# Optimization experiments

Hardware: AMD Instinct MI355X
Metric: run time of the kernel (lower is better)

The kernel has to match this reference:

```python
import jax, jax.numpy as jnp
import numpy as np
from jax import lax

EPS = 1e-5
NF, NH, HD = 1024, 2, 2  # num_features, heads, head_size (hidden_size=4)


def _prelu(x, a):
    return jnp.where(x >= 0, x, a * x)


def _bn2d(x, g, b):  # training-mode BatchNorm2d over (N,H,W)
    m = x.mean(axis=(0, 2, 3), keepdims=True)
    v = ((x - m) ** 2).mean(axis=(0, 2, 3), keepdims=True)
    return (x - m) / jnp.sqrt(v + EPS) * g[None, :, None, None] + b[None, :, None, None]


def _bn1d(x, g, b):  # training-mode BatchNorm1d over batch
    m = x.mean(axis=0, keepdims=True)
    v = ((x - m) ** 2).mean(axis=0, keepdims=True)
    return (x - m) / jnp.sqrt(v + EPS) * g + b


def _ln(x, g, b):
    m = x.mean(axis=-1, keepdims=True)
    v = ((x - m) ** 2).mean(axis=-1, keepdims=True)
    return (x - m) / jnp.sqrt(v + EPS) * g + b


def _conv(x, w, b, stride):
    y = lax.conv_general_dilated(x, w, window_strides=stride, padding='VALID',
                                 dimension_numbers=('NCHW', 'OIHW', 'NCHW'))
    return y + b[None, :, None, None]


def setup_inputs() -> dict:
    key = jax.random.key(0)
    ks = jax.random.split(key, 24)
    r = lambda i, shape, s=0.05: jax.random.normal(ks[i], shape, jnp.float32) * s
    ones = lambda n: jnp.ones((n,), jnp.float32)
    zeros = lambda n: jnp.zeros((n,), jnp.float32)
    return {
        'vertex_pos': r(0, (32, 3), 1.0),
        'body_mesh': r(1, (32, 20813, 3), 1.0),
        'conv1_w': r(2, (3, 1, 409, 3)), 'conv1_b': r(3, (3,)),
        'bn1_g': ones(3), 'bn1_b': zeros(3),
        'conv2_w': r(4, (3, 1, 330, 3)), 'conv2_b': r(5, (3,)),
        'bn2_g': ones(3), 'bn2_b': zeros(3),
        'prelu_a': jnp.float32(0.25),
        'wq': r(6, (4, 9)), 'bq': r(7, (4,)),
        'wk': r(8, (4, 9)), 'bk': r(9, (4,)),
        'wv': r(10, (4, 9)), 'bv': r(11, (4,)),
        'fc_w': r(12, (1024, 4096)), 'fc_b': r(13, (1024,)),
        'ff1_w': r(14, (1024, 1024)), 'ff1_b': r(15, (1024,)),
        'ln_g': ones(1024), 'ln_b': zeros(1024),
        'ff2_w': r(16, (48, 1024)), 'ff2_b': r(17, (48,)),
        'fus_w0': r(18, (48, 32, 3)), 'fus_b0': r(19, (48, 32)),
        'fus_w1': r(20, (48, 128, 32)), 'fus_b1': r(21, (48, 128)),
        'bnf0_g': ones(32), 'bnf0_b': zeros(32),
        'bnf1_g': ones(128), 'bnf1_b': zeros(128),
        'prelu_f': jnp.float32(0.25),
        'out_w': r(22, (1, 128)), 'out_b': r(23, (1,)),
    }


def reference(vertex_pos, body_mesh, conv1_w, conv1_b, bn1_g, bn1_b, conv2_w, conv2_b,
              bn2_g, bn2_b, prelu_a, wq, bq, wk, bk, wv, bv, fc_w, fc_b,
              ff1_w, ff1_b, ln_g, ln_b, ff2_w, ff2_b,
              fus_w0, fus_b0, fus_w1, fus_b1, bnf0_g, bnf0_b, bnf1_g, bnf1_b,
              prelu_f, out_w, out_b):
    B = vertex_pos.shape[0]
    # --- mesh encoder (MultiHeadAttention_conv.mesh_encoder) ---
    mesh = body_mesh.reshape(B, 1, -1, 3)                             # [B,1,20813,3]
    x = _bn2d(_conv(mesh, conv1_w, conv1_b, (6, 1)), bn1_g, bn1_b)    # [B,3,3401,1]
    x = x.reshape(B, 1, -1, 3)                                        # [B,1,3401,3]
    x = _bn2d(_conv(x, conv2_w, conv2_b, (1, 1)), bn2_g, bn2_b)       # [B,3,3072,1]
    x = _prelu(x.reshape(B, NF, -1), prelu_a)                         # [B,1024,9]
    # --- multi-head attention ---
    def heads(t):  # [B,NF,NH*HD] -> [B,NH,NF,HD]
        return t.reshape(B, NF, NH, HD).transpose(0, 2, 1, 3)
    q = heads(x @ wq.T + bq)
    k = heads(x @ wk.T + bk)
    v = heads(x @ wv.T + bv)
    scores = jnp.einsum('bhqd,bhkd->bhqk', q, k) / (HD ** 0.5)        # [B,2,1024,1024]
    attn = jax.nn.softmax(scores, axis=-1)
    av = jnp.einsum('bhqk,bhkd->bhqd', attn, v)
    av = av.transpose(0, 2, 1, 3).reshape(B, NF * NH * HD)            # [B,4096]
    h = av @ fc_w.T + fc_b                                            # [B,1024]
    # --- GMW feed-forward (residual) + motion weights ---
    h = h + jax.nn.elu(_ln(h @ ff1_w.T + ff1_b, ln_g, ln_b))
    mw = h @ ff2_w.T + ff2_b                                          # [B,48]
    w = mw / jnp.sum(mw, axis=1, keepdims=True)                       # normalized gates
    # --- fused MoE stage: 48 experts per depth, batched as one grouped GEMM ---
    s = vertex_pos.reshape(B, 3)
    for We, be, g, bb in ((fus_w0, fus_b0, bnf0_g, bnf0_b),
                          (fus_w1, fus_b1, bnf1_g, bnf1_b)):
        y = jnp.einsum('eoi,bi->beo', We, s) + be[None]               # [B,48,out]
        s = jnp.einsum('beo,be->bo', y, w)                            # gated sum over experts
        s = _prelu(_bn1d(s, g, bb), prelu_f)
    return jax.nn.sigmoid(s @ out_w.T + out_b)                        # [B,1]
```

## Files before the change

### kernel.cpp

```cpp
#include <hip/hip_runtime.h>

#define EPSF 1e-5f

__device__ __forceinline__ float wred(float v) {
#pragma unroll
  for (int off = 32; off > 0; off >>= 1) v += __shfl_down(v, off, 64);
  return v;
}

__global__ __launch_bounds__(256) void k_conv1(
    const float* __restrict__ mesh, const float* __restrict__ cw,
    const float* __restrict__ cb, float* __restrict__ out,
    float* __restrict__ part) {
  __shared__ float wsm[3684];
  __shared__ float sm[3513];
  __shared__ float pm[384];
  __shared__ float redm[4][6];
  const int tid = threadIdx.x;
  const int tile = blockIdx.x % 27, b = blockIdx.x / 27;
  const int oh0 = tile << 7;
  const int nvalid = min(128, 3401 - oh0);
  const int nload = (nvalid - 1) * 18 + 1227;
  for (int j = tid; j < 3681; j += 256) {
    int c = (j >= 2454) ? 2 : ((j >= 1227) ? 1 : 0);
    wsm[c * 1228 + (j - c * 1227)] = cw[j];
  }
  const float* src = mesh + b * 62439 + oh0 * 18;
  for (int j = tid; j < nload; j += 256) sm[j] = src[j];
  __syncthreads();
  const int half = tid >> 7, oidx = tid & 127;
  const float* xp = sm + oidx * 18;
  const int i0 = half ? 614 : 0, i1 = half ? 1226 : 614;
  float a0 = 0.f, a1 = 0.f, a2 = 0.f;
#pragma unroll 4
  for (int i = i0; i < i1; i += 2) {
    float2 x = *(const float2*)(xp + i);
    float2 w0 = *(const float2*)(wsm + i);
    float2 w1 = *(const float2*)(wsm + 1228 + i);
    float2 w2 = *(const float2*)(wsm + 2456 + i);
    a0 = fmaf(w0.x, x.x, fmaf(w0.y, x.y, a0));
    a1 = fmaf(w1.x, x.x, fmaf(w1.y, x.y, a1));
    a2 = fmaf(w2.x, x.x, fmaf(w2.y, x.y, a2));
  }
  if (half) {
    float x = xp[1226];
    a0 = fmaf(wsm[1226], x, a0);
    a1 = fmaf(wsm[1228 + 1226], x, a1);
    a2 = fmaf(wsm[2456 + 1226], x, a2);
    pm[oidx] = a0; pm[128 + oidx] = a1; pm[256 + oidx] = a2;
  }
  __syncthreads();
  float st[6] = {0.f, 0.f, 0.f, 0.f, 0.f, 0.f};
  if (!half && oidx < nvalid) {
    a0 += pm[oidx] + cb[0];
    a1 += pm[128 + oidx] + cb[1];
    a2 += pm[256 + oidx] + cb[2];
    float* op = out + b * 10203 + oh0 + oidx;
    op[0] = a0; op[3401] = a1; op[6802] = a2;
    st[0] = a0; st[1] = a0 * a0; st[2] = a1; st[3] = a1 * a1; st[4] = a2; st[5] = a2 * a2;
  }
  const int lane = tid & 63, wid = tid >> 6;
#pragma unroll
  for (int c = 0; c < 6; ++c) {
    float rv = wred(st[c]);
    if (lane == 0) redm[wid][c] = rv;
  }
  __syncthreads();
  if (tid < 6)
    part[blockIdx.x * 6 + tid] = redm[0][tid] + redm[1][tid] + redm[2][tid] + redm[3][tid];
}

__global__ __launch_bounds__(256) void k_conv2(
    const float* __restrict__ x1, const float* __restrict__ part1,
    const float* __restrict__ g1, const float* __restrict__ be1,
    const float* __restrict__ cw, const float* __restrict__ cb,
    float* __restrict__ out, float* __restrict__ part) {
  __shared__ float wsm[2970];
  __shared__ float sm[1371];
  __shared__ float pm[384];
  __shared__ float redm[4][6];
  __shared__ float coef[6];
  const int tid = threadIdx.x;
  const int lane = tid & 63, wid = tid >> 6;
  {
    float r[6] = {0.f, 0.f, 0.f, 0.f, 0.f, 0.f};
    for (int j = tid; j < 864; j += 256) {
#pragma unroll
      for (int c = 0; c < 6; ++c) r[c] += part1[j * 6 + c];
    }
#pragma unroll
    for (int c = 0; c < 6; ++c) {
      float rv = wred(r[c]);
      if (lane == 0) redm[wid][c] = rv;
    }
    __syncthreads();
    if (tid == 0) {
      const float inv_n = 1.f / (32.f * 3401.f);
#pragma unroll
      for (int c = 0; c < 3; ++c) {
        float s = redm[0][2 * c] + redm[1][2 * c] + redm[2][2 * c] + redm[3][2 * c];
        float ss = redm[0][2 * c + 1] + redm[1][2 * c + 1] + redm[2][2 * c + 1] + redm[3][2 * c + 1];
        float m = s * inv_n;
        float var = ss * inv_n - m * m;
        float a = g1[c] * rsqrtf(var + EPSF);
        coef[c] = a; coef[3 + c] = be1[c] - m * a;
      }
    }
  }
  for (int j = tid; j < 2970; j += 256) wsm[j] = cw[j];
  __syncthreads();
  const int tile = blockIdx.x % 24, b = blockIdx.x / 24;
  const int oh0 = tile << 7;
  const int g0 = oh0 * 3;
  const float* src = x1 + b * 10203 + g0;
  for (int j = tid; j < 1371; j += 256) {
    int gg = g0 + j;
    int c = (gg >= 6802) ? 2 : ((gg >= 3401) ? 1 : 0);
    sm[j] = fmaf(coef[c], src[j], coef[3 + c]);
  }
  __syncthreads();
  const int half = tid >> 7, oidx = tid & 127;
  const float* xp = sm + oidx * 3;
  const int i0 = half ? 496 : 0, i1 = half ? 990 : 496;
  float a0 = 0.f, a1 = 0.f, a2 = 0.f;
#pragma unroll 4
  for (int i = i0; i < i1; i += 2) {
    float x0 = xp[i], x1v = xp[i + 1];
    float2 w0 = *(const float2*)(wsm + i);
    float2 w1 = *(const float2*)(wsm + 990 + i);
    float2 w2 = *(const float2*)(wsm + 1980 + i);
    a0 = fmaf(w0.x, x0, fmaf(w0.y, x1v, a0));
    a1 = fmaf(w1.x, x0, fmaf(w1.y, x1v, a1));
    a2 = fmaf(w2.x, x0, fmaf(w2.y, x1v, a2));
  }
  if (half) { pm[oidx] = a0; pm[128 + oidx] = a1; pm[256 + oidx] = a2; }
  __syncthreads();
  float st[6] = {0.f, 0.f, 0.f, 0.f, 0.f, 0.f};
  if (!half) {
    a0 += pm[oidx] + cb[0];
    a1 += pm[128 + oidx] + cb[1];
    a2 += pm[256 + oidx] + cb[2];
    float* op = out + b * 9216 + oh0 + oidx;
    op[0] = a0; op[3072] = a1; op[6144] = a2;
    st[0] = a0; st[1] = a0 * a0; st[2] = a1; st[3] = a1 * a1; st[4] = a2; st[5] = a2 * a2;
  }
  __syncthreads();
#pragma unroll
  for (int c = 0; c < 6; ++c) {
    float rv = wred(st[c]);
    if (lane == 0) redm[wid][c] = rv;
  }
  __syncthreads();
  if (tid < 6)
    part[blockIdx.x * 6 + tid] = redm[0][tid] + redm[1][tid] + redm[2][tid] + redm[3][tid];
}

__global__ __launch_bounds__(256) void k_qkv(
    const float* __restrict__ x2, const float* __restrict__ part2,
    const float* __restrict__ g2, const float* __restrict__ be2,
    const float* __restrict__ pa_p,
    const float* __restrict__ wq, const float* __restrict__ bq,
    const float* __restrict__ wk, const float* __restrict__ bk,
    const float* __restrict__ wv, const float* __restrict__ bv,
    float* __restrict__ qo, float* __restrict__ ko, float* __restrict__ vo) {
  __shared__ float redm[4][6];
  __shared__ float coef[6];
  const int tid = threadIdx.x;
  const int lane = tid & 63, wid = tid >> 6;
  {
    float r[6] = {0.f, 0.f, 0.f, 0.f, 0.f, 0.f};
    for (int j = tid; j < 768; j += 256) {
#pragma unroll
      for (int c = 0; c < 6; ++c) r[c] += part2[j * 6 + c];
    }
#pragma unroll
    for (int c = 0; c < 6; ++c) {
      float rv = wred(r[c]);
      if (lane == 0) redm[wid][c] = rv;
    }
    __syncthreads();
    if (tid == 0) {
      const float inv_n = 1.f / (32.f * 3072.f);
#pragma unroll
      for (int c = 0; c < 3; ++c) {
        float s = redm[0][2 * c] + redm[1][2 * c] + redm[2][2 * c] + redm[3][2 * c];
        float ss = redm[0][2 * c + 1] + redm[1][2 * c + 1] + redm[2][2 * c + 1] + redm[3][2 * c + 1];
        float m = s * inv_n;
        float var = ss * inv_n - m * m;
        float a = g2[c] * rsqrtf(var + EPSF);
        coef[c] = a; coef[3 + c] = be2[c] - m * a;
      }
    }
    __syncthreads();
  }
  const float pa = pa_p[0];
  const int id = blockIdx.x * 256 + tid;
  const int b = id >> 10, f = id & 1023;
  const float* src = x2 + b * 9216 + f * 9;
  float x[9];
  const int z0 = f * 9;
#pragma unroll
  for (int j = 0; j < 9; ++j) {
    int z = z0 + j;
    int c = (z >= 6144) ? 2 : ((z >= 3072) ? 1 : 0);
    float v = fmaf(coef[c], src[j], coef[3 + c]);
    x[j] = (v >= 0.f) ? v : pa * v;
  }
  const float QSCALE = 0.70710678118654752f * 1.44269504088896341f;
#pragma unroll
  for (int dd = 0; dd < 4; ++dd) {
    float q = bq[dd], k = bk[dd], v = bv[dd];
#pragma unroll
    for (int j = 0; j < 9; ++j) {
      q = fmaf(wq[dd * 9 + j], x[j], q);
      k = fmaf(wk[dd * 9 + j], x[j], k);
      v = fmaf(wv[dd * 9 + j], x[j], v);
    }
    int hh = dd >> 1, d = dd & 1;
    int idx = ((b * 2 + hh) * 1024 + f) * 2 + d;
    qo[idx] = q * QSCALE;
    ko[idx] = k;
    vo[idx] = v;
  }
}

__device__ __forceinline__ int kvIdx(int j) { return j + (j >> 7); }

__global__ __launch_bounds__(256) void k_attn(
    const float* __restrict__ q, const float* __restrict__ k,
    const float* __restrict__ v, float* __restrict__ av) {
  __shared__ float4 kv[1032];
  __shared__ float smax[4];
  const int tid = threadIdx.x;
  const int bh = blockIdx.x >> 3, rblk = blockIdx.x & 7;
  const float2* kp = (const float2*)(k + bh * 2048);
  const float2* vp = (const float2*)(v + bh * 2048);
  float nkm = 0.f;
  for (int j = tid; j < 1024; j += 256) {
    float2 kk = kp[j], vv = vp[j];
    kv[kvIdx(j)] = make_float4(kk.x, kk.y, vv.x, vv.y);
    nkm = fmaxf(nkm, fmaf(kk.x, kk.x, kk.y * kk.y));
  }
#pragma unroll
  for (int off = 32; off > 0; off >>= 1) nkm = fmaxf(nkm, __shfl_xor(nkm, off, 64));
  if ((tid & 63) == 0) smax[tid >> 6] = nkm;
  __syncthreads();
  const float knorm = sqrtf(fmaxf(fmaxf(smax[0], smax[1]), fmaxf(smax[2], smax[3])));
  const int lane = tid & 63, w = tid >> 6;
  const int rg = (w << 3) | (lane >> 3);
  const int ks = lane & 7;
  const int r0 = rblk * 128 + rg * 4;
  const float4 q01 = *(const float4*)(q + (bh * 1024 + r0) * 2);
  const float4 q23 = *(const float4*)(q + (bh * 1024 + r0) * 2 + 4);
  float qx[4] = {q01.x, q01.z, q23.x, q23.z};
  float qy[4] = {q01.y, q01.w, q23.y, q23.w};
  float m[4], l[4] = {0.f, 0.f, 0.f, 0.f};
  float o0[4] = {0.f, 0.f, 0.f, 0.f}, o1[4] = {0.f, 0.f, 0.f, 0.f};
#pragma unroll
  for (int r = 0; r < 4; ++r) m[r] = sqrtf(fmaf(qx[r], qx[r], qy[r] * qy[r])) * knorm;
  const int j0 = ks * 128;
#pragma unroll 4
  for (int jj = 0; jj < 128; ++jj) {
    float4 kk = kv[kvIdx(j0 + jj)];
#pragma unroll
    for (int r = 0; r < 4; ++r) {
      float s = fmaf(qx[r], kk.x, qy[r] * kk.y);
      float p = exp2f(s - m[r]);
      l[r] += p;
      o0[r] = fmaf(p, kk.z, o0[r]);
      o1[r] = fmaf(p, kk.w, o1[r]);
    }
  }
#pragma unroll
  for (int off = 1; off <= 4; off <<= 1) {
#pragma unroll
    for (int r = 0; r < 4; ++r) {
      l[r] += __shfl_xor(l[r], off, 64);
      o0[r] += __shfl_xor(o0[r], off, 64);
      o1[r] += __shfl_xor(o1[r], off, 64);
    }
  }
  if (ks == 0) {
    const int b = bh >> 1, hh = bh & 1;
#pragma unroll
    for (int r = 0; r < 4; ++r) {
      float rl = 1.f / l[r];
      *(float2*)(av + b * 4096 + (r0 + r) * 4 + hh * 2) = make_float2(o0[r] * rl, o1[r] * rl);
    }
  }
}

__global__ __launch_bounds__(256) void k_fc(
    const float* __restrict__ x, const float* __restrict__ w,
    float* __restrict__ pout) {
  __shared__ float xs[128 * 36];
  const int tid = threadIdx.x;
  const int ob = blockIdx.x & 7, ksp = blockIdx.x >> 3;
  const int k0 = ksp * 128, obase = ob * 128;
  for (int r = tid; r < 4096; r += 256) {
    int b = r >> 7, kk = r & 127;
    xs[kk * 36 + b] = x[b * 4096 + k0 + kk];
  }
  __syncthreads();
  const int og = tid & 31, bg = tid >> 5;
  const int o = obase + og * 4, bb0 = bg * 4;
  float acc[4][4] = {};
  const float* wp = w + o * 4096 + k0;
  for (int kk = 0; kk < 128; kk += 4) {
    float4 x0 = *(const float4*)&xs[(kk + 0) * 36 + bb0];
    float4 x1 = *(const float4*)&xs[(kk + 1) * 36 + bb0];
    float4 x2 = *(const float4*)&xs[(kk + 2) * 36 + bb0];
    float4 x3 = *(const float4*)&xs[(kk + 3) * 36 + bb0];
#pragma unroll
    for (int oo = 0; oo < 4; ++oo) {
      float4 wv = *(const float4*)(wp + oo * 4096 + kk);
      acc[oo][0] = fmaf(wv.x, x0.x, fmaf(wv.y, x1.x, fmaf(wv.z, x2.x, fmaf(wv.w, x3.x, acc[oo][0]))));
      acc[oo][1] = fmaf(wv.x, x0.y, fmaf(wv.y, x1.y, fmaf(wv.z, x2.y, fmaf(wv.w, x3.y, acc[oo][1]))));
      acc[oo][2] = fmaf(wv.x, x0.z, fmaf(wv.y, x1.z, fmaf(wv.z, x2.z, fmaf(wv.w, x3.z, acc[oo][2]))));
      acc[oo][3] = fmaf(wv.x, x0.w, fmaf(wv.y, x1.w, fmaf(wv.z, x2.w, fmaf(wv.w, x3.w, acc[oo][3]))));
    }
  }
#pragma unroll
  for (int bi = 0; bi < 4; ++bi) {
    float4 rv = make_float4(acc[0][bi], acc[1][bi], acc[2][bi], acc[3][bi]);
    *(float4*)&pout[(ksp * 32 + bb0 + bi) * 1024 + o] = rv;
  }
}

__global__ __launch_bounds__(256) void k_ff1(
    const float* __restrict__ pfc, const float* __restrict__ fcb,
    const float* __restrict__ w, float* __restrict__ pout) {
  __shared__ float xs[64 * 36];
  const int tid = threadIdx.x;
  const int ob = blockIdx.x & 7, ksp = blockIdx.x >> 3;
  const int k0 = ksp * 64, obase = ob * 128;
  for (int r = tid; r < 2048; r += 256) {
    int b = r >> 6, kk = r & 63;
    float hv = fcb[k0 + kk];
#pragma unroll 4
    for (int j = 0; j < 32; ++j) hv += pfc[(j * 32 + b) * 1024 + k0 + kk];
    xs[kk * 36 + b] = hv;
  }
  __syncthreads();
  const int og = tid & 31, bg = tid >> 5;
  const int o = obase + og * 4, bb0 = bg * 4;
  float acc[4][4] = {};
  const float* wp = w + o * 1024 + k0;
  for (int kk = 0; kk < 64; kk += 4) {
    float4 x0 = *(const float4*)&xs[(kk + 0) * 36 + bb0];
    float4 x1 = *(const float4*)&xs[(kk + 1) * 36 + bb0];
    float4 x2 = *(const float4*)&xs[(kk + 2) * 36 + bb0];
    float4 x3 = *(const float4*)&xs[(kk + 3) * 36 + bb0];
#pragma unroll
    for (int oo = 0; oo < 4; ++oo) {
      float4 wv = *(const float4*)(wp + oo * 1024 + kk);
      acc[oo][0] = fmaf(wv.x, x0.x, fmaf(wv.y, x1.x, fmaf(wv.z, x2.x, fmaf(wv.w, x3.x, acc[oo][0]))));
      acc[oo][1] = fmaf(wv.x, x0.y, fmaf(wv.y, x1.y, fmaf(wv.z, x2.y, fmaf(wv.w, x3.y, acc[oo][1]))));
      acc[oo][2] = fmaf(wv.x, x0.z, fmaf(wv.y, x1.z, fmaf(wv.z, x2.z, fmaf(wv.w, x3.z, acc[oo][2]))));
      acc[oo][3] = fmaf(wv.x, x0.w, fmaf(wv.y, x1.w, fmaf(wv.z, x2.w, fmaf(wv.w, x3.w, acc[oo][3]))));
    }
  }
#pragma unroll
  for (int bi = 0; bi < 4; ++bi) {
    float4 rv = make_float4(acc[0][bi], acc[1][bi], acc[2][bi], acc[3][bi]);
    *(float4*)&pout[(ksp * 32 + bb0 + bi) * 1024 + o] = rv;
  }
}

__global__ __launch_bounds__(256) void k_tail1(
    const float* __restrict__ pfc, const float* __restrict__ fcb,
    const float* __restrict__ pff1, const float* __restrict__ ff1b,
    const float* __restrict__ lng, const float* __restrict__ lnb,
    const float* __restrict__ f2w, const float* __restrict__ f2b,
    const float* __restrict__ vp, const float* __restrict__ w0,
    const float* __restrict__ b0, float* __restrict__ wgate,
    float* __restrict__ s1pre) {
  __shared__ float hs[1024], ts[1024];
  __shared__ float mw_s[48];
  __shared__ float red2[4][2];
  __shared__ float bc[2];
  __shared__ float tot_s;
  const int b = blockIdx.x, tid = threadIdx.x;
  const int lane = tid & 63, wid = tid >> 6;
  for (int o = tid; o < 1024; o += 256) {
    float hv = fcb[o];
#pragma unroll 4
    for (int j = 0; j < 32; ++j) hv += pfc[(j * 32 + b) * 1024 + o];
    hs[o] = hv;
    float tv = ff1b[o];
#pragma unroll 4
    for (int j = 0; j < 16; ++j) tv += pff1[(j * 32 + b) * 1024 + o];
    ts[o] = tv;
  }
  __syncthreads();
  float ls = 0.f, lss = 0.f;
  for (int o = tid; o < 1024; o += 256) {
    float t = ts[o];
    ls += t; lss += t * t;
  }
  ls = wred(ls); lss = wred(lss);
  if (lane == 0) { red2[wid][0] = ls; red2[wid][1] = lss; }
  __syncthreads();
  if (tid == 0) {
    float S = red2[0][0] + red2[1][0] + red2[2][0] + red2[3][0];
    float SS = red2[0][1] + red2[1][1] + red2[2][1] + red2[3][1];
    float m = S * (1.f / 1024.f);
    float var = SS * (1.f / 1024.f) - m * m;
    bc[0] = m; bc[1] = rsqrtf(var + EPSF);
  }
  __syncthreads();
  const float m = bc[0], inv = bc[1];
  for (int o = tid; o < 1024; o += 256) {
    float y = fmaf((ts[o] - m) * inv, lng[o], lnb[o]);
    float e = (y > 0.f) ? y : expm1f(y);
    ts[o] = hs[o] + e;
  }
  __syncthreads();
  if (tid < 192) {
    int e = tid >> 2, part = tid & 3;
    float acc = 0.f;
    const float* wr = f2w + e * 1024 + part * 4;
    for (int i = 0; i < 64; ++i) {
      float4 wv = *(const float4*)(wr + i * 16);
      int ob = i * 16 + part * 4;
      acc = fmaf(wv.x, ts[ob], fmaf(wv.y, ts[ob + 1], fmaf(wv.z, ts[ob + 2], fmaf(wv.w, ts[ob + 3], acc))));
    }
    acc += __shfl_down(acc, 1, 64);
    acc += __shfl_down(acc, 2, 64);
    if (part == 0) mw_s[e] = acc + f2b[e];
  }
  __syncthreads();
  if (tid < 64) {
    float v = (tid < 48) ? mw_s[tid] : 0.f;
    float t = wred(v);
    if (tid == 0) tot_s = t;
  }
  __syncthreads();
  if (tid < 48) {
    float wg = mw_s[tid] / tot_s;
    mw_s[tid] = wg;
    wgate[b * 48 + tid] = wg;
  }
  __syncthreads();
  if (tid < 32) {
    const int o = tid;
    const float v0 = vp[b * 3], v1 = vp[b * 3 + 1], v2 = vp[b * 3 + 2];
    float acc = 0.f;
#pragma unroll 4
    for (int e = 0; e < 48; ++e) {
      const float* wr = w0 + (e * 32 + o) * 3;
      float y = b0[e * 32 + o] + wr[0] * v0 + wr[1] * v1 + wr[2] * v2;
      acc = fmaf(mw_s[e], y, acc);
    }
    s1pre[b * 32 + o] = acc;
  }
}

__global__ __launch_bounds__(128) void k_moe1(
    const float* __restrict__ s1pre, const float* __restrict__ g0,
    const float* __restrict__ be0, const float* __restrict__ pf_p,
    const float* __restrict__ wgate, const float* __restrict__ w1,
    const float* __restrict__ b1, float* __restrict__ s2pre) {
  __shared__ float s1n[32];
  __shared__ float wg[48];
  const int b = blockIdx.x, tid = threadIdx.x;
  const float pf = pf_p[0];
  if (tid < 48) wg[tid] = wgate[b * 48 + tid];
  if (tid < 32) {
    const int o = tid;
    float s = 0.f, ss = 0.f;
    for (int bb = 0; bb < 32; ++bb) {
      float v = s1pre[bb * 32 + o];
      s += v; ss += v * v;
    }
    float mm = s * (1.f / 32.f);
    float var = ss * (1.f / 32.f) - mm * mm;
    float a = g0[o] * rsqrtf(var + EPSF);
    float c = be0[o] - mm * a;
    float v = fmaf(s1pre[b * 32 + o], a, c);
    s1n[o] = (v >= 0.f) ? v : pf * v;
  }
  __syncthreads();
  const int op = tid;
  float acc = 0.f;
  for (int e = 0; e < 48; ++e) {
    const float* wr = w1 + (e * 128 + op) * 32;
    float y = b1[e * 128 + op];
#pragma unroll
    for (int i = 0; i < 32; i += 4) {
      float4 wv = *(const float4*)(wr + i);
      y = fmaf(wv.x, s1n[i], fmaf(wv.y, s1n[i + 1], fmaf(wv.z, s1n[i + 2], fmaf(wv.w, s1n[i + 3], y))));
    }
    acc = fmaf(wg[e], y, acc);
  }
  s2pre[b * 128 + op] = acc;
}

__global__ __launch_bounds__(256) void k_final(
    const float* __restrict__ s2pre, const float* __restrict__ g1,
    const float* __restrict__ be1, const float* __restrict__ pf_p,
    const float* __restrict__ ow, const float* __restrict__ obp,
    float* __restrict__ outp) {
  __shared__ float s2[32 * 132];
  __shared__ float ca[128], cb[128];
  const int tid = threadIdx.x;
  for (int r = tid; r < 4096; r += 256) {
    int b = r >> 7, o = r & 127;
    s2[b * 132 + o] = s2pre[r];
  }
  __syncthreads();
  if (tid < 128) {
    const int o = tid;
    float s = 0.f, ss = 0.f;
    for (int b = 0; b < 32; ++b) {
      float v = s2[b * 132 + o];
      s += v; ss += v * v;
    }
    float mm = s * (1.f / 32.f);
    float var = ss * (1.f / 32.f) - mm * mm;
    float a = g1[o] * rsqrtf(var + EPSF);
    ca[o] = a; cb[o] = be1[o] - mm * a;
  }
  __syncthreads();
  const float pf = pf_p[0];
  if (tid < 32) {
    const int b = tid;
    float acc = 0.f;
#pragma unroll 4
    for (int o = 0; o < 128; ++o) {
      float v = fmaf(s2[b * 132 + o], ca[o], cb[o]);
      v = (v >= 0.f) ? v : pf * v;
      acc = fmaf(v, ow[o], acc);
    }
    float z = acc + obp[0];
    outp[b] = 1.f / (1.f + __expf(-z));
  }
}

extern "C" void kernel_launch(void* const* d_in, const int* in_sizes, int n_in,
                              void* d_out, int out_size, void* d_ws, size_t ws_size,
                              hipStream_t stream) {
  (void)in_sizes; (void)n_in; (void)out_size; (void)ws_size;
  const float* vertex_pos = (const float*)d_in[0];
  const float* body_mesh  = (const float*)d_in[1];
  const float* conv1_w    = (const float*)d_in[2];
  const float* conv1_b    = (const float*)d_in[3];
  const float* bn1_g      = (const float*)d_in[4];
  const float* bn1_b      = (const float*)d_in[5];
  const float* conv2_w    = (const float*)d_in[6];
  const float* conv2_b    = (const float*)d_in[7];
  const float* bn2_g      = (const float*)d_in[8];
  const float* bn2_b      = (const float*)d_in[9];
  const float* prelu_a    = (const float*)d_in[10];
  const float* wq = (const float*)d_in[11]; const float* bq = (const float*)d_in[12];
  const float* wk = (const float*)d_in[13]; const float* bk = (const float*)d_in[14];
  const float* wv = (const float*)d_in[15]; const float* bv = (const float*)d_in[16];
  const float* fc_w  = (const float*)d_in[17]; const float* fc_b  = (const float*)d_in[18];
  const float* ff1_w = (const float*)d_in[19]; const float* ff1_b = (const float*)d_in[20];
  const float* ln_g  = (const float*)d_in[21]; const float* ln_b  = (const float*)d_in[22];
  const float* ff2_w = (const float*)d_in[23]; const float* ff2_b = (const float*)d_in[24];
  const float* fus_w0 = (const float*)d_in[25]; const float* fus_b0 = (const float*)d_in[26];
  const float* fus_w1 = (const float*)d_in[27]; const float* fus_b1 = (const float*)d_in[28];
  const float* bnf0_g = (const float*)d_in[29]; const float* bnf0_b = (const float*)d_in[30];
  const float* bnf1_g = (const float*)d_in[31]; const float* bnf1_b = (const float*)d_in[32];
  const float* prelu_f = (const float*)d_in[33];
  const float* out_w = (const float*)d_in[34]; const float* out_b = (const float*)d_in[35];

  float* ws = (float*)d_ws;
  float* conv1_out = ws + 0;
  float* conv2_out = ws + 326496;
  float* qws = ws + 621408;
  float* kws = ws + 752480;
  float* vws = ws + 883552;
  float* p_fc = ws + 0;
  float* av    = ws + 1048576;
  float* p_ff1 = ws + 1179648;
  float* part1 = ws + 1703936;
  float* part2 = ws + 1709120;
  float* wgate = ws + 1713728;
  float* s1pre = ws + 1715264;
  float* s2pre = ws + 1716288;

  k_conv1<<<864, 256, 0, stream>>>(body_mesh, conv1_w, conv1_b, conv1_out, part1);
  k_conv2<<<768, 256, 0, stream>>>(conv1_out, part1, bn1_g, bn1_b, conv2_w, conv2_b, conv2_out, part2);
  k_qkv<<<128, 256, 0, stream>>>(conv2_out, part2, bn2_g, bn2_b, prelu_a,
                                 wq, bq, wk, bk, wv, bv, qws, kws, vws);
  k_attn<<<512, 256, 0, stream>>>(qws, kws, vws, av);
  k_fc<<<256, 256, 0, stream>>>(av, fc_w, p_fc);
  k_ff1<<<128, 256, 0, stream>>>(p_fc, fc_b, ff1_w, p_ff1);
  k_tail1<<<32, 256, 0, stream>>>(p_fc, fc_b, p_ff1, ff1_b, ln_g, ln_b, ff2_w, ff2_b,
                                  vertex_pos, fus_w0, fus_b0, wgate, s1pre);
  k_moe1<<<32, 128, 0, stream>>>(s1pre, bnf0_g, bnf0_b, prelu_f, wgate, fus_w1, fus_b1, s2pre);
  k_final<<<1, 256, 0, stream>>>(s2pre, bnf1_g, bnf1_b, prelu_f, out_w, out_b, (float*)d_out);
}
```

Measured before the change: 372.1 us.

## Register-tile conv kernels over outputs, split FC/FF1 finer, add h-reduction kernel

```diff
diff --git a/kernel.cpp b/kernel.cpp
--- a/kernel.cpp
+++ b/kernel.cpp
@@ -14,7 +14,8 @@
     float* __restrict__ part) {
   __shared__ float wsm[3684];
   __shared__ float sm[3513];
-  __shared__ float pm[384];
+  __shared__ float red[3072];
+  __shared__ float pm2[384];
   __shared__ float redm[4][6];
   const int tid = threadIdx.x;
   const int tile = blockIdx.x % 27, b = blockIdx.x / 27;
@@ -28,36 +29,60 @@
   const float* src = mesh + b * 62439 + oh0 * 18;
   for (int j = tid; j < nload; j += 256) sm[j] = src[j];
   __syncthreads();
-  const int half = tid >> 7, oidx = tid & 127;
-  const float* xp = sm + oidx * 18;
-  const int i0 = half ? 614 : 0, i1 = half ? 1226 : 614;
-  float a0 = 0.f, a1 = 0.f, a2 = 0.f;
-#pragma unroll 4
-  for (int i = i0; i < i1; i += 2) {
-    float2 x = *(const float2*)(xp + i);
+  const int kc = tid >> 5, s = tid & 31;
+  const int i0 = kc * 154, i1 = min(1227, i0 + 154);
+  float acc[4][3] = {};
+  const float* xb = sm + s * 18;
+  int i = i0;
+#pragma unroll 2
+  for (; i + 1 < i1; i += 2) {
     float2 w0 = *(const float2*)(wsm + i);
     float2 w1 = *(const float2*)(wsm + 1228 + i);
     float2 w2 = *(const float2*)(wsm + 2456 + i);
-    a0 = fmaf(w0.x, x.x, fmaf(w0.y, x.y, a0));
-    a1 = fmaf(w1.x, x.x, fmaf(w1.y, x.y, a1));
-    a2 = fmaf(w2.x, x.x, fmaf(w2.y, x.y, a2));
-  }
-  if (half) {
-    float x = xp[1226];
-    a0 = fmaf(wsm[1226], x, a0);
-    a1 = fmaf(wsm[1228 + 1226], x, a1);
-    a2 = fmaf(wsm[2456 + 1226], x, a2);
-    pm[oidx] = a0; pm[128 + oidx] = a1; pm[256 + oidx] = a2;
+#pragma unroll
+    for (int r = 0; r < 4; ++r) {
+      float2 x = *(const float2*)(xb + r * 576 + i);
+      acc[r][0] = fmaf(w0.x, x.x, fmaf(w0.y, x.y, acc[r][0]));
+      acc[r][1] = fmaf(w1.x, x.x, fmaf(w1.y, x.y, acc[r][1]));
+      acc[r][2] = fmaf(w2.x, x.x, fmaf(w2.y, x.y, acc[r][2]));
+    }
+  }
+  if (i < i1) {
+    float w0 = wsm[i], w1 = wsm[1228 + i], w2 = wsm[2456 + i];
+#pragma unroll
+    for (int r = 0; r < 4; ++r) {
+      float x = xb[r * 576 + i];
+      acc[r][0] = fmaf(w0, x, acc[r][0]);
+      acc[r][1] = fmaf(w1, x, acc[r][1]);
+      acc[r][2] = fmaf(w2, x, acc[r][2]);
+    }
+  }
+#pragma unroll
+  for (int r = 0; r < 4; ++r)
+#pragma unroll
+    for (int ch = 0; ch < 3; ++ch)
+      red[kc * 384 + s * 12 + r * 3 + ch] = acc[r][ch];
+  __syncthreads();
+  float v0 = cb[tid % 3];
+#pragma unroll
+  for (int c2 = 0; c2 < 8; ++c2) v0 += red[c2 * 384 + tid];
+  pm2[tid] = v0;
+  if (tid < 128) {
+    float v1 = cb[(tid + 256) % 3];
+#pragma unroll
+    for (int c2 = 0; c2 < 8; ++c2) v1 += red[c2 * 384 + tid + 256];
+    pm2[tid + 256] = v1;
   }
   __syncthreads();
   float st[6] = {0.f, 0.f, 0.f, 0.f, 0.f, 0.f};
-  if (!half && oidx < nvalid) {
-    a0 += pm[oidx] + cb[0];
-    a1 += pm[128 + oidx] + cb[1];
-    a2 += pm[256 + oidx] + cb[2];
-    float* op = out + b * 10203 + oh0 + oidx;
-    op[0] = a0; op[3401] = a1; op[6802] = a2;
-    st[0] = a0; st[1] = a0 * a0; st[2] = a1; st[3] = a1 * a1; st[4] = a2; st[5] = a2 * a2;
+  if (tid < 128 && tid < nvalid) {
+    const int s2 = tid & 31, r2 = tid >> 5;
+    float y0 = pm2[s2 * 12 + r2 * 3 + 0];
+    float y1 = pm2[s2 * 12 + r2 * 3 + 1];
+    float y2 = pm2[s2 * 12 + r2 * 3 + 2];
+    float* op = out + b * 10203 + oh0 + tid;
+    op[0] = y0; op[3401] = y1; op[6802] = y2;
+    st[0] = y0; st[1] = y0 * y0; st[2] = y1; st[3] = y1 * y1; st[4] = y2; st[5] = y2 * y2;
   }
   const int lane = tid & 63, wid = tid >> 6;
 #pragma unroll
@@ -75,9 +100,10 @@
     const float* __restrict__ g1, const float* __restrict__ be1,
     const float* __restrict__ cw, const float* __restrict__ cb,
     float* __restrict__ out, float* __restrict__ part) {
-  __shared__ float wsm[2970];
+  __shared__ float wsm[2976];
   __shared__ float sm[1371];
-  __shared__ float pm[384];
+  __shared__ float red[3072];
+  __shared__ float pm2[384];
   __shared__ float redm[4][6];
   __shared__ float coef[6];
   const int tid = threadIdx.x;
@@ -107,7 +133,10 @@
       }
     }
   }
-  for (int j = tid; j < 2970; j += 256) wsm[j] = cw[j];
+  for (int j = tid; j < 2970; j += 256) {
+    int c = (j >= 1980) ? 2 : ((j >= 990) ? 1 : 0);
+    wsm[c * 992 + (j - c * 990)] = cw[j];
+  }
   __syncthreads();
   const int tile = blockIdx.x % 24, b = blockIdx.x / 24;
   const int oh0 = tile << 7;
@@ -119,32 +148,51 @@
     sm[j] = fmaf(coef[c], src[j], coef[3 + c]);
   }
   __syncthreads();
-  const int half = tid >> 7, oidx = tid & 127;
-  const float* xp = sm + oidx * 3;
-  const int i0 = half ? 496 : 0, i1 = half ? 990 : 496;
-  float a0 = 0.f, a1 = 0.f, a2 = 0.f;
-#pragma unroll 4
-  for (int i = i0; i < i1; i += 2) {
-    float x0 = xp[i], x1v = xp[i + 1];
+  const int kc = tid >> 5, s = tid & 31;
+  const int i0 = kc * 124, i1 = min(990, i0 + 124);
+  float acc[4][3] = {};
+  const float* xb = sm + s * 3;
+  int i = i0;
+#pragma unroll 2
+  for (; i + 1 < i1; i += 2) {
     float2 w0 = *(const float2*)(wsm + i);
-    float2 w1 = *(const float2*)(wsm + 990 + i);
-    float2 w2 = *(const float2*)(wsm + 1980 + i);
-    a0 = fmaf(w0.x, x0, fmaf(w0.y, x1v, a0));
-    a1 = fmaf(w1.x, x0, fmaf(w1.y, x1v, a1));
-    a2 = fmaf(w2.x, x0, fmaf(w2.y, x1v, a2));
-  }
-  if (half) { pm[oidx] = a0; pm[128 + oidx] = a1; pm[256 + oidx] = a2; }
+    float2 w1 = *(const float2*)(wsm + 992 + i);
+    float2 w2 = *(const float2*)(wsm + 1984 + i);
+#pragma unroll
+    for (int r = 0; r < 4; ++r) {
+      float2 x = *(const float2*)(xb + r * 96 + i);
+      acc[r][0] = fmaf(w0.x, x.x, fmaf(w0.y, x.y, acc[r][0]));
+      acc[r][1] = fmaf(w1.x, x.x, fmaf(w1.y, x.y, acc[r][1]));
+      acc[r][2] = fmaf(w2.x, x.x, fmaf(w2.y, x.y, acc[r][2]));
+    }
+  }
+#pragma unroll
+  for (int r = 0; r < 4; ++r)
+#pragma unroll
+    for (int ch = 0; ch < 3; ++ch)
+      red[kc * 384 + s * 12 + r * 3 + ch] = acc[r][ch];
+  __syncthreads();
+  float v0 = cb[tid % 3];
+#pragma unroll
+  for (int c2 = 0; c2 < 8; ++c2) v0 += red[c2 * 384 + tid];
+  pm2[tid] = v0;
+  if (tid < 128) {
+    float v1 = cb[(tid + 256) % 3];
+#pragma unroll
+    for (int c2 = 0; c2 < 8; ++c2) v1 += red[c2 * 384 + tid + 256];
+    pm2[tid + 256] = v1;
+  }
   __syncthreads();
   float st[6] = {0.f, 0.f, 0.f, 0.f, 0.f, 0.f};
-  if (!half) {
-    a0 += pm[oidx] + cb[0];
-    a1 += pm[128 + oidx] + cb[1];
-    a2 += pm[256 + oidx] + cb[2];
-    float* op = out + b * 9216 + oh0 + oidx;
-    op[0] = a0; op[3072] = a1; op[6144] = a2;
-    st[0] = a0; st[1] = a0 * a0; st[2] = a1; st[3] = a1 * a1; st[4] = a2; st[5] = a2 * a2;
-  }
-  __syncthreads();
+  if (tid < 128) {
+    const int s2 = tid & 31, r2 = tid >> 5;
+    float y0 = pm2[s2 * 12 + r2 * 3 + 0];
+    float y1 = pm2[s2 * 12 + r2 * 3 + 1];
+    float y2 = pm2[s2 * 12 + r2 * 3 + 2];
+    float* op = out + b * 9216 + oh0 + tid;
+    op[0] = y0; op[3072] = y1; op[6144] = y2;
+    st[0] = y0; st[1] = y0 * y0; st[2] = y1; st[3] = y1 * y1; st[4] = y2; st[5] = y2 * y2;
+  }
 #pragma unroll
   for (int c = 0; c < 6; ++c) {
     float rv = wred(st[c]);
@@ -295,81 +343,85 @@
     float* __restrict__ pout) {
   __shared__ float xs[128 * 36];
   const int tid = threadIdx.x;
-  const int ob = blockIdx.x & 7, ksp = blockIdx.x >> 3;
-  const int k0 = ksp * 128, obase = ob * 128;
+  const int ob = blockIdx.x & 15, ksp = blockIdx.x >> 4;
+  const int k0 = ksp * 128, obase = ob * 64;
   for (int r = tid; r < 4096; r += 256) {
     int b = r >> 7, kk = r & 127;
     xs[kk * 36 + b] = x[b * 4096 + k0 + kk];
   }
   __syncthreads();
-  const int og = tid & 31, bg = tid >> 5;
-  const int o = obase + og * 4, bb0 = bg * 4;
-  float acc[4][4] = {};
+  const int og = tid & 15, bg = tid >> 4;
+  const int o = obase + og * 4, bb0 = bg * 2;
+  float acc[4][2] = {};
   const float* wp = w + o * 4096 + k0;
   for (int kk = 0; kk < 128; kk += 4) {
-    float4 x0 = *(const float4*)&xs[(kk + 0) * 36 + bb0];
-    float4 x1 = *(const float4*)&xs[(kk + 1) * 36 + bb0];
-    float4 x2 = *(const float4*)&xs[(kk + 2) * 36 + bb0];
-    float4 x3 = *(const float4*)&xs[(kk + 3) * 36 + bb0];
+    float2 x0 = *(const float2*)&xs[(kk + 0) * 36 + bb0];
+    float2 x1 = *(const float2*)&xs[(kk + 1) * 36 + bb0];
+    float2 x2 = *(const float2*)&xs[(kk + 2) * 36 + bb0];
+    float2 x3 = *(const float2*)&xs[(kk + 3) * 36 + bb0];
 #pragma unroll
     for (int oo = 0; oo < 4; ++oo) {
       float4 wv = *(const float4*)(wp + oo * 4096 + kk);
       acc[oo][0] = fmaf(wv.x, x0.x, fmaf(wv.y, x1.x, fmaf(wv.z, x2.x, fmaf(wv.w, x3.x, acc[oo][0]))));
       acc[oo][1] = fmaf(wv.x, x0.y, fmaf(wv.y, x1.y, fmaf(wv.z, x2.y, fmaf(wv.w, x3.y, acc[oo][1]))));
-      acc[oo][2] = fmaf(wv.x, x0.z, fmaf(wv.y, x1.z, fmaf(wv.z, x2.z, fmaf(wv.w, x3.z, acc[oo][2]))));
-      acc[oo][3] = fmaf(wv.x, x0.w, fmaf(wv.y, x1.w, fmaf(wv.z, x2.w, fmaf(wv.w, x3.w, acc[oo][3]))));
-    }
-  }
-#pragma unroll
-  for (int bi = 0; bi < 4; ++bi) {
+    }
+  }
+#pragma unroll
+  for (int bi = 0; bi < 2; ++bi) {
     float4 rv = make_float4(acc[0][bi], acc[1][bi], acc[2][bi], acc[3][bi]);
     *(float4*)&pout[(ksp * 32 + bb0 + bi) * 1024 + o] = rv;
   }
 }
 
+__global__ __launch_bounds__(256) void k_hred(
+    const float* __restrict__ pfc, const float* __restrict__ fcb,
+    float* __restrict__ h) {
+  const int idx = blockIdx.x * 256 + threadIdx.x;
+  const int b = idx >> 10, o = idx & 1023;
+  float hv = fcb[o];
+#pragma unroll 4
+  for (int j = 0; j < 32; ++j) hv += pfc[(j * 32 + b) * 1024 + o];
+  h[idx] = hv;
+}
+
 __global__ __launch_bounds__(256) void k_ff1(
-    const float* __restrict__ pfc, const float* __restrict__ fcb,
-    const float* __restrict__ w, float* __restrict__ pout) {
+    const float* __restrict__ h, const float* __restrict__ w,
+    float* __restrict__ pout) {
   __shared__ float xs[64 * 36];
   const int tid = threadIdx.x;
-  const int ob = blockIdx.x & 7, ksp = blockIdx.x >> 3;
-  const int k0 = ksp * 64, obase = ob * 128;
+  const int ob = blockIdx.x & 15, ksp = blockIdx.x >> 4;
+  const int k0 = ksp * 64, obase = ob * 64;
   for (int r = tid; r < 2048; r += 256) {
     int b = r >> 6, kk = r & 63;
-    float hv = fcb[k0 + kk];
-#pragma unroll 4
-    for (int j = 0; j < 32; ++j) hv += pfc[(j * 32 + b) * 1024 + k0 + kk];
-    xs[kk * 36 + b] = hv;
-  }
-  __syncthreads();
-  const int og = tid & 31, bg = tid >> 5;
-  const int o = obase + og * 4, bb0 = bg * 4;
-  float acc[4][4] = {};
+    xs[kk * 36 + b] = h[b * 1024 + k0 + kk];
+  }
+  __syncthreads();
+  const int og = tid & 15, bg = tid >> 4;
+  const int o = obase + og * 4, bb0 = bg * 2;
+  float acc[4][2] = {};
   const float* wp = w + o * 1024 + k0;
   for (int kk = 0; kk < 64; kk += 4) {
-    float4 x0 = *(const float4*)&xs[(kk + 0) * 36 + bb0];
-    float4 x1 = *(const float4*)&xs[(kk + 1) * 36 + bb0];
-    float4 x2 = *(const float4*)&xs[(kk + 2) * 36 + bb0];
-    float4 x3 = *(const float4*)&xs[(kk + 3) * 36 + bb0];
+    float2 x0 = *(const float2*)&xs[(kk + 0) * 36 + bb0];
+    float2 x1 = *(const float2*)&xs[(kk + 1) * 36 + bb0];
+    float2 x2 = *(const float2*)&xs[(kk + 2) * 36 + bb0];
+    float2 x3 = *(const float2*)&xs[(kk + 3) * 36 + bb0];
 #pragma unroll
     for (int oo = 0; oo < 4; ++oo) {
       float4 wv = *(const float4*)(wp + oo * 1024 + kk);
       acc[oo][0] = fmaf(wv.x, x0.x, fmaf(wv.y, x1.x, fmaf(wv.z, x2.x, fmaf(wv.w, x3.x, acc[oo][0]))));
       acc[oo][1] = fmaf(wv.x, x0.y, fmaf(wv.y, x1.y, fmaf(wv.z, x2.y, fmaf(wv.w, x3.y, acc[oo][1]))));
-      acc[oo][2] = fmaf(wv.x, x0.z, fmaf(wv.y, x1.z, fmaf(wv.z, x2.z, fmaf(wv.w, x3.z, acc[oo][2]))));
-      acc[oo][3] = fmaf(wv.x, x0.w, fmaf(wv.y, x1.w, fmaf(wv.z, x2.w, fmaf(wv.w, x3.w, acc[oo][3]))));
-    }
-  }
-#pragma unroll
-  for (int bi = 0; bi < 4; ++bi) {
+    }
+  }
+#pragma unroll
+  for (int bi = 0; bi < 2; ++bi) {
     float4 rv = make_float4(acc[0][bi], acc[1][bi], acc[2][bi], acc[3][bi]);
     *(float4*)&pout[(ksp * 32 + bb0 + bi) * 1024 + o] = rv;
   }
 }
 
 __global__ __launch_bounds__(256) void k_tail1(
-    const float* __restrict__ pfc, const float* __restrict__ fcb,
-    const float* __restrict__ pff1, const float* __restrict__ ff1b,
+    const float* __restrict__ h, const float* __restrict__ pff1,
+    const float* __restrict__ ff1b,
     const float* __restrict__ lng, const float* __restrict__ lnb,
     const float* __restrict__ f2w, const float* __restrict__ f2b,
     const float* __restrict__ vp, const float* __restrict__ w0,
@@ -383,10 +435,7 @@
   const int b = blockIdx.x, tid = threadIdx.x;
   const int lane = tid & 63, wid = tid >> 6;
   for (int o = tid; o < 1024; o += 256) {
-    float hv = fcb[o];
-#pragma unroll 4
-    for (int j = 0; j < 32; ++j) hv += pfc[(j * 32 + b) * 1024 + o];
-    hs[o] = hv;
+    hs[o] = h[b * 1024 + o];
     float tv = ff1b[o];
 #pragma unroll 4
     for (int j = 0; j < 16; ++j) tv += pff1[(j * 32 + b) * 1024 + o];
@@ -574,21 +623,23 @@
   float* vws = ws + 883552;
   float* p_fc = ws + 0;
   float* av    = ws + 1048576;
-  float* p_ff1 = ws + 1179648;
-  float* part1 = ws + 1703936;
-  float* part2 = ws + 1709120;
-  float* wgate = ws + 1713728;
-  float* s1pre = ws + 1715264;
-  float* s2pre = ws + 1716288;
+  float* hbuf  = ws + 1179648;
+  float* p_ff1 = ws + 1212416;
+  float* part1 = ws + 1736704;
+  float* part2 = ws + 1741888;
+  float* wgate = ws + 1746496;
+  float* s1pre = ws + 1748032;
+  float* s2pre = ws + 1749056;
 
   k_conv1<<<864, 256, 0, stream>>>(body_mesh, conv1_w, conv1_b, conv1_out, part1);
   k_conv2<<<768, 256, 0, stream>>>(conv1_out, part1, bn1_g, bn1_b, conv2_w, conv2_b, conv2_out, part2);
   k_qkv<<<128, 256, 0, stream>>>(conv2_out, part2, bn2_g, bn2_b, prelu_a,
                                  wq, bq, wk, bk, wv, bv, qws, kws, vws);
   k_attn<<<512, 256, 0, stream>>>(qws, kws, vws, av);
-  k_fc<<<256, 256, 0, stream>>>(av, fc_w, p_fc);
-  k_ff1<<<128, 256, 0, stream>>>(p_fc, fc_b, ff1_w, p_ff1);
-  k_tail1<<<32, 256, 0, stream>>>(p_fc, fc_b, p_ff1, ff1_b, ln_g, ln_b, ff2_w, ff2_b,
+  k_fc<<<512, 256, 0, stream>>>(av, fc_w, p_fc);
+  k_hred<<<128, 256, 0, stream>>>(p_fc, fc_b, hbuf);
+  k_ff1<<<256, 256, 0, stream>>>(hbuf, ff1_w, p_ff1);
+  k_tail1<<<32, 256, 0, stream>>>(hbuf, p_ff1, ff1_b, ln_g, ln_b, ff2_w, ff2_b,
                                   vertex_pos, fus_w0, fus_b0, wgate, s1pre);
   k_moe1<<<32, 128, 0, stream>>>(s1pre, bnf0_g, bnf0_b, prelu_f, wgate, fus_w1, fus_b1, s2pre);
   k_final<<<1, 256, 0, stream>>>(s2pre, bnf1_g, bnf1_b, prelu_f, out_w, out_b, (float*)d_out);
```

After: 418.8 us. 1.13x slower.
